# Kernel tuning notes

Hardware: AMD Instinct MI355X
Metric: run time of the kernel (lower is better)

Reference implementation:

```python
import jax, jax.numpy as jnp
import numpy as np

D_MODEL = 1024
N_HEADS = 16
D_HEAD = D_MODEL // N_HEADS


def setup_inputs() -> dict:
    key = jax.random.key(0)
    k1, k2, k3 = jax.random.split(key, 3)
    B, T = 4, 2048
    x = jax.random.normal(k1, (B, T, D_MODEL), dtype=jnp.float32)
    # torch nn.Linear weights: (out_features, in_features), scaled init
    w_qkv = jax.random.normal(k2, (3 * D_MODEL, D_MODEL), dtype=jnp.float32) / np.sqrt(D_MODEL)
    w_out = jax.random.normal(k3, (D_MODEL, D_MODEL), dtype=jnp.float32) / np.sqrt(D_MODEL)
    return {"x": x, "w_qkv": w_qkv, "w_out": w_out}


def reference(x, w_qkv, w_out):
    B, T, _ = x.shape
    qkv = jnp.einsum('btd,ed->bte', x, w_qkv)  # (B,T,3*d_model)
    q, k, v = jnp.split(qkv, 3, axis=-1)
    # (B,T,H,dh) -> (B,H,T,dh)
    def heads(t):
        return t.reshape(B, T, N_HEADS, D_HEAD).transpose(0, 2, 1, 3)
    q, k, v = heads(q), heads(k), heads(v)
    scores = jnp.einsum('bhqd,bhkd->bhqk', q, k) / jnp.sqrt(jnp.float32(D_HEAD))
    causal = jnp.tril(jnp.ones((T, T), dtype=bool))  # True = keep
    scores = jnp.where(causal, scores, -jnp.inf)
    weights = jax.nn.softmax(scores, axis=-1)
    out = jnp.einsum('bhqk,bhkd->bhqd', weights, v)
    out = out.transpose(0, 2, 1, 3).reshape(B, T, D_MODEL)
    return jnp.einsum('btd,ed->bte', out, w_out)
```

## Files before the change

### kernel.cpp

```cpp
#include <hip/hip_runtime.h>

typedef __attribute__((ext_vector_type(8))) short short8;
typedef __attribute__((ext_vector_type(4))) float f32x4;
typedef __attribute__((ext_vector_type(4))) unsigned short us4;
typedef unsigned short u16;

#define MFMA16(a, b, c) __builtin_amdgcn_mfma_f32_16x16x32_bf16(a, b, c, 0, 0, 0)

static __device__ __forceinline__ u16 f2bf(float f) {
  union { float f; unsigned u; } v; v.f = f;
  unsigned r = v.u + 0x7fffu + ((v.u >> 16) & 1u);
  return (u16)(r >> 16);
}

static __device__ __forceinline__ unsigned cvtpk(float lo, float hi) {
  unsigned r;
  asm("v_cvt_pk_bf16_f32 %0, %1, %2" : "=v"(r) : "v"(lo), "v"(hi));
  return r;
}

static __device__ __forceinline__ void gl_lds16(const u16* g, u16* l) {
  __builtin_amdgcn_global_load_lds((const __attribute__((address_space(1))) void*)g,
                                   (__attribute__((address_space(3))) void*)l,
                                   16, 0, 0);
}

__global__ __launch_bounds__(256)
void cvt_bf16(const float* __restrict__ src, u16* __restrict__ dst, int n8)
{
  int i = blockIdx.x * 256 + threadIdx.x;
  const int stride = gridDim.x * 256;
  for (; i < n8; i += stride) {
    f32x4 a = ((const f32x4*)src)[2 * i];
    f32x4 b = ((const f32x4*)src)[2 * i + 1];
    short8 o;
    o[0] = (short)f2bf(a[0]); o[1] = (short)f2bf(a[1]);
    o[2] = (short)f2bf(a[2]); o[3] = (short)f2bf(a[3]);
    o[4] = (short)f2bf(b[0]); o[5] = (short)f2bf(b[1]);
    o[6] = (short)f2bf(b[2]); o[7] = (short)f2bf(b[3]);
    ((short8*)dst)[i] = o;
  }
}

template<int MODE>
__global__ __launch_bounds__(256)
void gemm_bt(const u16* __restrict__ A, const u16* __restrict__ B,
             u16* __restrict__ outp, float* __restrict__ outf)
{
  __shared__ u16 Ash[128 * 32];
  __shared__ u16 Bsh[128 * 32];
  const int tid = threadIdx.x;
  const int lane = tid & 63;
  const int l15 = lane & 15, g = lane >> 4;
  const int w = tid >> 6;
  const int wr = w >> 1, wc = w & 1;
  const long m0 = (long)blockIdx.x * 128;
  const long n0 = (long)blockIdx.y * 128;

  f32x4 acc[4][4] = {};

  const int c0 = tid, c1 = tid + 256;
  const long arow0 = m0 + (c0 >> 2), arow1 = m0 + (c1 >> 2);
  const u16* pa0;
  const u16* pa1;
  if (MODE == 2) {
    int b0 = (int)(arow0 >> 11), t0 = (int)(arow0 & 2047);
    int b1 = (int)(arow1 >> 11), t1 = (int)(arow1 & 2047);
    pa0 = A + (size_t)(b0 * 16) * 131072u + (size_t)t0 * 64u + (c0 & 3) * 8;
    pa1 = A + (size_t)(b1 * 16) * 131072u + (size_t)t1 * 64u + (c1 & 3) * 8;
  } else {
    pa0 = A + arow0 * 1024 + (c0 & 3) * 8;
    pa1 = A + arow1 * 1024 + (c1 & 3) * 8;
  }
  const u16* pb0 = B + (n0 + (c0 >> 2)) * 1024 + (c0 & 3) * 8;
  const u16* pb1 = B + (n0 + (c1 >> 2)) * 1024 + (c1 & 3) * 8;
  u16* la0 = Ash + c0 * 8;
  u16* la1 = Ash + c1 * 8;
  u16* lb0 = Bsh + c0 * 8;
  u16* lb1 = Bsh + c1 * 8;

  const u16* afp[4];
  const u16* bfp[4];
  #pragma unroll
  for (int mi = 0; mi < 4; ++mi)
    afp[mi] = &Ash[(wr * 64 + mi * 16 + l15) * 32 + g * 8];
  #pragma unroll
  for (int ni = 0; ni < 4; ++ni)
    bfp[ni] = &Bsh[(wc * 64 + ni * 16 + l15) * 32 + g * 8];

  for (int k0 = 0; k0 < 1024; k0 += 32) {
    __syncthreads();
    gl_lds16(pa0, la0); gl_lds16(pa1, la1);
    gl_lds16(pb0, lb0); gl_lds16(pb1, lb1);
    if (MODE == 2) {
      long d = (k0 & 32) ? (131072 - 32) : 32;
      pa0 += d; pa1 += d;
    } else {
      pa0 += 32; pa1 += 32;
    }
    pb0 += 32; pb1 += 32;
    __syncthreads();

    short8 af[4], bf[4];
    #pragma unroll
    for (int mi = 0; mi < 4; ++mi) af[mi] = *(const short8*)afp[mi];
    #pragma unroll
    for (int ni = 0; ni < 4; ++ni) bf[ni] = *(const short8*)bfp[ni];
    #pragma unroll
    for (int mi = 0; mi < 4; ++mi)
      #pragma unroll
      for (int ni = 0; ni < 4; ++ni)
        acc[mi][ni] = MFMA16(af[mi], bf[ni], acc[mi][ni]);
  }

  if (MODE == 2) {
    #pragma unroll
    for (int mi = 0; mi < 4; ++mi) {
      long m = m0 + wr * 64 + mi * 16 + g * 4;
      #pragma unroll
      for (int ni = 0; ni < 4; ++ni) {
        int n = (int)n0 + wc * 64 + ni * 16 + l15;
        #pragma unroll
        for (int r = 0; r < 4; ++r)
          outf[(m + r) * 1024 + n] = acc[mi][ni][r];
      }
    }
  } else {
    #pragma unroll
    for (int mi = 0; mi < 4; ++mi) {
      long m = m0 + wr * 64 + mi * 16 + g * 4;
      int b = (int)(m >> 11);
      int t = (int)(m & 2047);
      #pragma unroll
      for (int ni = 0; ni < 4; ++ni) {
        int e = (int)n0 + wc * 64 + ni * 16 + l15;
        int sel = e >> 10;
        int ee = e & 1023;
        int h = ee >> 6, dh = ee & 63;
        size_t bh131k = (size_t)(b * 16 + h) * 131072u;
        if (sel < 2) {
          float sc = (sel == 0) ? 0.125f : 1.0f;
          size_t base = (size_t)sel * 8388608u + bh131k + (size_t)t * 64u + dh;
          #pragma unroll
          for (int r = 0; r < 4; ++r)
            outp[base + (size_t)r * 64u] = f2bf(acc[mi][ni][r] * sc);
        } else {
          size_t base = 16777216u + bh131k + (size_t)dh * 2048u + (size_t)t;
          us4 v;
          #pragma unroll
          for (int r = 0; r < 4; ++r) v[r] = f2bf(acc[mi][ni][r]);
          *(us4*)&outp[base] = v;
        }
      }
    }
  }
}

__global__ __launch_bounds__(256, 4)
void attn(const u16* __restrict__ Q, const u16* __restrict__ K,
          const u16* __restrict__ VT, u16* __restrict__ O)
{
  __shared__ u16 Ksh[2][64 * 64];
  __shared__ u16 Vsh[2][64 * 64];
  __shared__ u16 Psh[4][16 * 64];

  const int tid = threadIdx.x;
  const int lane = tid & 63;
  const int l15 = lane & 15, g = lane >> 4;
  const int w = tid >> 6;
  const int bid = blockIdx.x;
  const int qi = 15 - (bid >> 6);
  const int bh = bid & 63;
  const int q0 = qi * 128;
  const int qb = q0 + w * 32;
  const int nt = qi * 2 + 2;

  const u16* Qp = Q + (size_t)bh * 131072u;
  const u16* Kp = K + (size_t)bh * 131072u;
  const u16* Vp = VT + (size_t)bh * 131072u;

  short8 qf[2][2];
  #pragma unroll
  for (int mi = 0; mi < 2; ++mi)
    #pragma unroll
    for (int kc = 0; kc < 2; ++kc)
      qf[mi][kc] = *(const short8*)&Qp[(qb + mi * 16 + l15) * 64 + kc * 32 + g * 8];

  f32x4 oacc[2][4] = {};
  float mrun[2] = {-1e30f, -1e30f};
  float lrun[2] = {0.f, 0.f};

  const int cA = tid, cB = tid + 256;
  const int rA = cA >> 3, uA = ((cA & 7) ^ (rA & 7)) * 8;
  const int rB = cB >> 3, uB = ((cB & 7) ^ (rB & 7)) * 8;

#define STAGE(kv0s, b) do {                                            \
    gl_lds16(Kp + ((kv0s) + rA) * 64 + uA, Ksh[b] + cA * 8);           \
    gl_lds16(Kp + ((kv0s) + rB) * 64 + uB, Ksh[b] + cB * 8);           \
    gl_lds16(Vp + (size_t)rA * 2048u + (kv0s) + uA, Vsh[b] + cA * 8);  \
    gl_lds16(Vp + (size_t)rB * 2048u + (kv0s) + uB, Vsh[b] + cB * 8);  \
  } while (0)

  STAGE(0, 0);
  int cur = 0;

  for (int ti = 0; ti < nt; ++ti) {
    const int kv0 = ti * 64;
    if (ti + 1 < nt) {
      STAGE(kv0 + 64, cur ^ 1);
      asm volatile("s_waitcnt vmcnt(4)" ::: "memory");
    } else {
      asm volatile("s_waitcnt vmcnt(0)" ::: "memory");
    }
    __builtin_amdgcn_s_barrier();
    __builtin_amdgcn_sched_barrier(0);

    if (kv0 <= qb + 31) {
      const u16* Kb = Ksh[cur];
      const u16* Vb = Vsh[cur];

      f32x4 s[2][4] = {};
      #pragma unroll
      for (int kc = 0; kc < 2; ++kc)
        #pragma unroll
        for (int ni = 0; ni < 4; ++ni) {
          int row = ni * 16 + l15;
          short8 kb = *(const short8*)&Kb[row * 64 + (((kc * 4 + g) ^ (row & 7)) << 3)];
          #pragma unroll
          for (int mi = 0; mi < 2; ++mi)
            s[mi][ni] = MFMA16(kb, qf[mi][kc], s[mi][ni]);
        }

      if (kv0 + 63 > qb) {
        #pragma unroll
        for (int mi = 0; mi < 2; ++mi) {
          int qv = qb + mi * 16 + l15;
          #pragma unroll
          for (int ni = 0; ni < 4; ++ni)
            #pragma unroll
            for (int r = 0; r < 4; ++r)
              if (kv0 + ni * 16 + g * 4 + r > qv)
                s[mi][ni][r] = -1e30f;
        }
      }

      float sc[2];
      #pragma unroll
      for (int mi = 0; mi < 2; ++mi) {
        float mx0 = fmaxf(fmaxf(s[mi][0][0], s[mi][0][1]),
                          fmaxf(s[mi][0][2], s[mi][0][3]));
        float mx1 = fmaxf(fmaxf(s[mi][1][0], s[mi][1][1]),
                          fmaxf(s[mi][1][2], s[mi][1][3]));
        float mx2 = fmaxf(fmaxf(s[mi][2][0], s[mi][2][1]),
                          fmaxf(s[mi][2][2], s[mi][2][3]));
        float mx3 = fmaxf(fmaxf(s[mi][3][0], s[mi][3][1]),
                          fmaxf(s[mi][3][2], s[mi][3][3]));
        float mx = fmaxf(fmaxf(mx0, mx1), fmaxf(mx2, mx3));
        mx = fmaxf(mx, __shfl_xor(mx, 16));
        mx = fmaxf(mx, __shfl_xor(mx, 32));
        float mn = fmaxf(mrun[mi], mx);
        sc[mi] = __expf(mrun[mi] - mn);
        mrun[mi] = mn;
        float rs = 0.f;
        #pragma unroll
        for (int ni = 0; ni < 4; ++ni)
          #pragma unroll
          for (int r = 0; r < 4; ++r) {
            float p = __expf(s[mi][ni][r] - mn);
            s[mi][ni][r] = p;
            rs += p;
          }
        rs += __shfl_xor(rs, 16);
        rs += __shfl_xor(rs, 32);
        lrun[mi] = lrun[mi] * sc[mi] + rs;
        #pragma unroll
        for (int nj = 0; nj < 4; ++nj) {
          oacc[mi][nj][0] *= sc[mi];
          oacc[mi][nj][1] *= sc[mi];
          oacc[mi][nj][2] *= sc[mi];
          oacc[mi][nj][3] *= sc[mi];
        }
      }

      u16* Pw = &Psh[w][0];
      short8 pb[2][2];
      #pragma unroll
      for (int mi = 0; mi < 2; ++mi) {
        #pragma unroll
        for (int ni = 0; ni < 4; ++ni) {
          int col = ni * 16 + g * 4;
          uint2 pv;
          pv.x = cvtpk(s[mi][ni][0], s[mi][ni][1]);
          pv.y = cvtpk(s[mi][ni][2], s[mi][ni][3]);
          *(uint2*)&Pw[l15 * 64 + (col ^ ((l15 & 7) << 3))] = pv;
        }
        #pragma unroll
        for (int kc = 0; kc < 2; ++kc)
          pb[mi][kc] = *(const short8*)&Pw[l15 * 64 + (((kc * 4 + g) ^ (l15 & 7)) << 3)];
      }

      #pragma unroll
      for (int kc = 0; kc < 2; ++kc)
        #pragma unroll
        for (int nj = 0; nj < 4; ++nj) {
          int vrow = nj * 16 + l15;
          short8 vb = *(const short8*)&Vb[vrow * 64 + (((kc * 4 + g) ^ (vrow & 7)) << 3)];
          #pragma unroll
          for (int mi = 0; mi < 2; ++mi)
            oacc[mi][nj] = MFMA16(vb, pb[mi][kc], oacc[mi][nj]);
        }
    }

    __builtin_amdgcn_sched_barrier(0);
    __builtin_amdgcn_s_barrier();
    cur ^= 1;
  }
#undef STAGE

  #pragma unroll
  for (int mi = 0; mi < 2; ++mi) {
    float inv = 1.0f / lrun[mi];
    int t = qb + mi * 16 + l15;
    size_t base = (size_t)bh * 131072u + (size_t)t * 64u;
    #pragma unroll
    for (int nj = 0; nj < 4; ++nj) {
      uint2 o;
      o.x = cvtpk(oacc[mi][nj][0] * inv, oacc[mi][nj][1] * inv);
      o.y = cvtpk(oacc[mi][nj][2] * inv, oacc[mi][nj][3] * inv);
      *(uint2*)&O[base + nj * 16 + g * 4] = o;
    }
  }
}

extern "C" void kernel_launch(void* const* d_in, const int* in_sizes, int n_in,
                              void* d_out, int out_size, void* d_ws, size_t ws_size,
                              hipStream_t stream)
{
  (void)in_sizes; (void)n_in; (void)out_size; (void)ws_size;
  const float* x    = (const float*)d_in[0];
  const float* wqkv = (const float*)d_in[1];
  const float* wout = (const float*)d_in[2];
  u16* ws  = (u16*)d_ws;
  u16* Qw   = ws;
  u16* Kw   = ws + 8388608;
  u16* VTw  = ws + 16777216;
  u16* wqb  = ws + 25165824;
  u16* wob  = ws + 28311552;
  u16* xb   = (u16*)d_out;
  float* y  = (float*)d_out;

  hipLaunchKernelGGL(cvt_bf16, dim3(2048), dim3(256), 0, stream, x,    xb,  1048576);
  hipLaunchKernelGGL(cvt_bf16, dim3(1536), dim3(256), 0, stream, wqkv, wqb, 393216);
  hipLaunchKernelGGL(cvt_bf16, dim3(512),  dim3(256), 0, stream, wout, wob, 131072);
  hipLaunchKernelGGL((gemm_bt<1>), dim3(64, 24), dim3(256), 0, stream, xb, wqb, ws, (float*)nullptr);
  hipLaunchKernelGGL(attn,         dim3(1024),   dim3(256), 0, stream, Qw, Kw, VTw, Qw);
  hipLaunchKernelGGL((gemm_bt<2>), dim3(64, 8),  dim3(256), 0, stream, Qw, wob, (u16*)nullptr, y);
}
```

Measured before the change: 198.7 us.

## Swizzle GEMM tiles per XCD, widen attention blocks, lazy softmax rescale

The GEMM grids become 1D with a block-to-tile mapping that groups tiles per XCD, so each XCD's L2 sees more reuse of A and B panels. The attention kernel moves to 512 threads and 256-query blocks, which halves K/V staging per query and spreads each tile load over more threads. It also skips the online-softmax rescale of the accumulator unless the running max grows by more than 8 for some lane. The trade-offs are higher register and LDS pressure per block, and exponentials that can be as large as e^8 before rescaling.

```diff
diff --git a/kernel.cpp b/kernel.cpp
--- a/kernel.cpp
+++ b/kernel.cpp
@@ -54,8 +54,20 @@
   const int l15 = lane & 15, g = lane >> 4;
   const int w = tid >> 6;
   const int wr = w >> 1, wc = w & 1;
-  const long m0 = (long)blockIdx.x * 128;
-  const long n0 = (long)blockIdx.y * 128;
+
+  const int bid = blockIdx.x;
+  const int xcd = bid & 7, idx = bid >> 3;
+  const int cx = xcd & 3, cy = xcd >> 2;
+  int mt, nt;
+  if (MODE == 1) {
+    mt = cx * 16 + (idx & 15);
+    nt = cy * 12 + (idx >> 4);
+  } else {
+    mt = cx * 16 + (idx & 15);
+    nt = cy * 4 + (idx >> 4);
+  }
+  const long m0 = (long)mt * 128;
+  const long n0 = (long)nt * 128;
 
   f32x4 acc[4][4] = {};
 
@@ -156,24 +168,24 @@
   }
 }
 
-__global__ __launch_bounds__(256, 4)
+__global__ __launch_bounds__(512, 4)
 void attn(const u16* __restrict__ Q, const u16* __restrict__ K,
           const u16* __restrict__ VT, u16* __restrict__ O)
 {
   __shared__ u16 Ksh[2][64 * 64];
   __shared__ u16 Vsh[2][64 * 64];
-  __shared__ u16 Psh[4][16 * 64];
+  __shared__ u16 Psh[8][16 * 64];
 
   const int tid = threadIdx.x;
   const int lane = tid & 63;
   const int l15 = lane & 15, g = lane >> 4;
   const int w = tid >> 6;
   const int bid = blockIdx.x;
-  const int qi = 15 - (bid >> 6);
+  const int qi = 7 - (bid >> 6);
   const int bh = bid & 63;
-  const int q0 = qi * 128;
+  const int q0 = qi * 256;
   const int qb = q0 + w * 32;
-  const int nt = qi * 2 + 2;
+  const int nt = qi * 4 + 4;
 
   const u16* Qp = Q + (size_t)bh * 131072u;
   const u16* Kp = K + (size_t)bh * 131072u;
@@ -190,15 +202,11 @@
   float mrun[2] = {-1e30f, -1e30f};
   float lrun[2] = {0.f, 0.f};
 
-  const int cA = tid, cB = tid + 256;
-  const int rA = cA >> 3, uA = ((cA & 7) ^ (rA & 7)) * 8;
-  const int rB = cB >> 3, uB = ((cB & 7) ^ (rB & 7)) * 8;
+  const int rA = tid >> 3, uA = ((tid & 7) ^ (rA & 7)) * 8;
 
 #define STAGE(kv0s, b) do {                                            \
-    gl_lds16(Kp + ((kv0s) + rA) * 64 + uA, Ksh[b] + cA * 8);           \
-    gl_lds16(Kp + ((kv0s) + rB) * 64 + uB, Ksh[b] + cB * 8);           \
-    gl_lds16(Vp + (size_t)rA * 2048u + (kv0s) + uA, Vsh[b] + cA * 8);  \
-    gl_lds16(Vp + (size_t)rB * 2048u + (kv0s) + uB, Vsh[b] + cB * 8);  \
+    gl_lds16(Kp + ((kv0s) + rA) * 64 + uA, Ksh[b] + tid * 8);          \
+    gl_lds16(Vp + (size_t)rA * 2048u + (kv0s) + uA, Vsh[b] + tid * 8); \
   } while (0)
 
   STAGE(0, 0);
@@ -208,7 +216,7 @@
     const int kv0 = ti * 64;
     if (ti + 1 < nt) {
       STAGE(kv0 + 64, cur ^ 1);
-      asm volatile("s_waitcnt vmcnt(4)" ::: "memory");
+      asm volatile("s_waitcnt vmcnt(2)" ::: "memory");
     } else {
       asm volatile("s_waitcnt vmcnt(0)" ::: "memory");
     }
@@ -244,7 +252,6 @@
         }
       }
 
-      float sc[2];
       #pragma unroll
       for (int mi = 0; mi < 2; ++mi) {
         float mx0 = fmaxf(fmaxf(s[mi][0][0], s[mi][0][1]),
@@ -258,9 +265,20 @@
         float mx = fmaxf(fmaxf(mx0, mx1), fmaxf(mx2, mx3));
         mx = fmaxf(mx, __shfl_xor(mx, 16));
         mx = fmaxf(mx, __shfl_xor(mx, 32));
-        float mn = fmaxf(mrun[mi], mx);
-        sc[mi] = __expf(mrun[mi] - mn);
-        mrun[mi] = mn;
+        if (!__all(mx - mrun[mi] <= 8.0f)) {
+          float mn = fmaxf(mrun[mi], mx);
+          float sc = __expf(mrun[mi] - mn);
+          mrun[mi] = mn;
+          lrun[mi] *= sc;
+          #pragma unroll
+          for (int nj = 0; nj < 4; ++nj) {
+            oacc[mi][nj][0] *= sc;
+            oacc[mi][nj][1] *= sc;
+            oacc[mi][nj][2] *= sc;
+            oacc[mi][nj][3] *= sc;
+          }
+        }
+        float mn = mrun[mi];
         float rs = 0.f;
         #pragma unroll
         for (int ni = 0; ni < 4; ++ni)
@@ -272,14 +290,7 @@
           }
         rs += __shfl_xor(rs, 16);
         rs += __shfl_xor(rs, 32);
-        lrun[mi] = lrun[mi] * sc[mi] + rs;
-        #pragma unroll
-        for (int nj = 0; nj < 4; ++nj) {
-          oacc[mi][nj][0] *= sc[mi];
-          oacc[mi][nj][1] *= sc[mi];
-          oacc[mi][nj][2] *= sc[mi];
-          oacc[mi][nj][3] *= sc[mi];
-        }
+        lrun[mi] += rs;
       }
 
       u16* Pw = &Psh[w][0];
@@ -352,7 +363,7 @@
   hipLaunchKernelGGL(cvt_bf16, dim3(2048), dim3(256), 0, stream, x,    xb,  1048576);
   hipLaunchKernelGGL(cvt_bf16, dim3(1536), dim3(256), 0, stream, wqkv, wqb, 393216);
   hipLaunchKernelGGL(cvt_bf16, dim3(512),  dim3(256), 0, stream, wout, wob, 131072);
-  hipLaunchKernelGGL((gemm_bt<1>), dim3(64, 24), dim3(256), 0, stream, xb, wqb, ws, (float*)nullptr);
-  hipLaunchKernelGGL(attn,         dim3(1024),   dim3(256), 0, stream, Qw, Kw, VTw, Qw);
-  hipLaunchKernelGGL((gemm_bt<2>), dim3(64, 8),  dim3(256), 0, stream, Qw, wob, (u16*)nullptr, y);
-}
+  hipLaunchKernelGGL((gemm_bt<1>), dim3(1536), dim3(256), 0, stream, xb, wqb, ws, (float*)nullptr);
+  hipLaunchKernelGGL(attn,         dim3(512),  dim3(512), 0, stream, Qw, Kw, VTw, Qw);
+  hipLaunchKernelGGL((gemm_bt<2>), dim3(512),  dim3(256), 0, stream, Qw, wob, (u16*)nullptr, y);
+}
```

After: 191.4 us. 1.04x faster.
